# Kernel tuning notes

Measured on AMD Instinct MI355X. Metric: run time of the kernel, lower is better.

Reference implementation:

```python
import jax, jax.numpy as jnp
import numpy as np

N_TOK, BATCH, D, MEM, H, W = 196, 64, 256, 2048, 16, 16


def setup_inputs() -> dict:
    key = jax.random.key(0)
    ks = jax.random.split(key, 9)
    w_scale = 1.0 / np.sqrt(D)  # ~ Linear default init scale
    return {
        "input_tokens": jax.random.normal(ks[0], (N_TOK, BATCH, D), jnp.float32),
        "ch_memory": jax.random.normal(ks[1], (MEM, D), jnp.float32) * 0.1,
        "ch_wq": jax.random.normal(ks[2], (D, D), jnp.float32) * w_scale,
        "ch_wk": jax.random.normal(ks[3], (D, D), jnp.float32) * w_scale,
        "ch_wv": jax.random.normal(ks[4], (D, D), jnp.float32) * w_scale,
        "sp_memory": jax.random.normal(ks[5], (MEM, H, W), jnp.float32) * 0.1,
        "sp_wq": jax.random.normal(ks[6], (D, D), jnp.float32) * w_scale,
        "sp_wk": jax.random.normal(ks[7], (D, D), jnp.float32) * w_scale,
        "sp_wv": jax.random.normal(ks[8], (D, D), jnp.float32) * w_scale,
    }


def reference(input_tokens, ch_memory, ch_wq, ch_wk, ch_wv,
              sp_memory, sp_wq, sp_wk, sp_wv):
    n_tok, batch, d = input_tokens.shape
    hw = d  # spatial branch requires feature_dim == H*W
    x = input_tokens.reshape(n_tok * batch, d)  # [NB, D]

    # ---- Channel memory branch: dot-product softmax read ----
    q = x @ ch_wq.T                       # [NB, D]
    k = ch_memory @ ch_wk.T               # [M, D]
    v = ch_memory @ ch_wv.T               # [M, D]
    scores = (q @ k.T) * (1.0 / jnp.sqrt(jnp.float32(d)))  # [NB, M]
    att_c = jax.nn.softmax(scores, axis=-1)
    out_c = att_c @ v                     # [NB, D]

    # ---- Spatial memory branch: SSIM-score softmax read ----
    mem_flat = sp_memory.reshape(sp_memory.shape[0], hw)  # [M, HW]
    qf = x @ sp_wq.T                      # [NB, HW]
    kf = mem_flat @ sp_wk.T               # [M, HW]
    vf = mem_flat @ sp_wv.T               # [M, HW]

    q_mean = jnp.mean(qf, axis=1, keepdims=True)          # [NB, 1]
    k_mean = jnp.mean(kf, axis=1, keepdims=True)          # [M, 1]
    q_var = jnp.var(qf, axis=1, ddof=1, keepdims=True)    # unbiased, like torch.var
    k_var = jnp.var(kf, axis=1, ddof=1, keepdims=True)
    cov = ((qf - q_mean) @ (kf - k_mean).T) / jnp.float32(hw - 1)  # [NB, M]

    c1, c2 = 0.01, 0.03
    mean_prod = q_mean @ k_mean.T                          # [NB, M]
    numerator = (2.0 * mean_prod + c1) * (2.0 * cov + c2)
    denominator = (q_mean ** 2 + (k_mean.T) ** 2 + c1) * (q_var + k_var.T + c2)
    ssim = numerator / (denominator + 1e-8)                # [NB, M]

    att_s = jax.nn.softmax(ssim, axis=-1)
    out_s = att_s @ vf                     # [NB, HW] == [NB, D]

    return (out_c + out_s).reshape(n_tok, batch, d)
```

## Files before the change

### kernel.cpp

```cpp
#include <hip/hip_runtime.h>

#define NBQ 12544
#define DM  256
#define MM  2048

typedef __attribute__((ext_vector_type(8)))  __bf16 bf16x8;
typedef __attribute__((ext_vector_type(4)))  float  floatx4;

__device__ __forceinline__ ushort f2bf(float x) {
    unsigned u = __float_as_uint(x);
    u += 0x7fffu + ((u >> 16) & 1u);
    return (ushort)(u >> 16);
}
__device__ __forceinline__ float bf2f(ushort h) {
    return __uint_as_float(((unsigned)h) << 16);
}

__device__ __forceinline__ void glds16(const ushort* g, ushort* l) {
    __builtin_amdgcn_global_load_lds(
        (const __attribute__((address_space(1))) unsigned int*)g,
        (__attribute__((address_space(3))) unsigned int*)l, 16, 0, 0);
}

__global__ __launch_bounds__(256) void gemm_proj_all(
    const float* __restrict__ x,      const float* __restrict__ ch_mem,
    const float* __restrict__ ch_wq,  const float* __restrict__ ch_wk,
    const float* __restrict__ ch_wv,  const float* __restrict__ sp_mem,
    const float* __restrict__ sp_wq,  const float* __restrict__ sp_wk,
    const float* __restrict__ sp_wv,
    ushort* __restrict__ Qb,  ushort* __restrict__ QFb,
    ushort* __restrict__ Kb,  ushort* __restrict__ KFb,
    ushort* __restrict__ Vtb, ushort* __restrict__ VFtb)
{
    __shared__ ushort As[64][72];
    __shared__ ushort W1s[64][72];
    __shared__ ushort W2s[64][72];

    int bid = blockIdx.x;
    const float* A; const float* W1; const float* W2;
    ushort* C1; ushort* C2; int nrows, trans2;
    if (bid < 784) {
        A = x; W1 = ch_wq; W2 = sp_wq; C1 = Qb; C2 = QFb; nrows = NBQ; trans2 = 0;
    } else if (bid < 912) {
        A = ch_mem; W1 = ch_wk; W2 = ch_wv; C1 = Kb; C2 = Vtb;
        nrows = MM; trans2 = 1; bid -= 784;
    } else {
        A = sp_mem; W1 = sp_wk; W2 = sp_wv; C1 = KFb; C2 = VFtb;
        nrows = MM; trans2 = 1; bid -= 912;
    }
    const int r0 = (bid >> 2) * 64;
    const int c0 = (bid & 3) * 64;

    const int tid  = threadIdx.x;
    const int wv   = tid >> 6;
    const int lane = tid & 63;
    const int quad = lane >> 4;
    const int l16  = lane & 15;
    const int rw = (wv & 1) * 32;
    const int cw = (wv >> 1) * 32;

    floatx4 acc1[2][2], acc2[2][2];
    #pragma unroll
    for (int i = 0; i < 2; ++i)
        #pragma unroll
        for (int j = 0; j < 2; ++j) {
            acc1[i][j] = (floatx4){0.f, 0.f, 0.f, 0.f};
            acc2[i][j] = (floatx4){0.f, 0.f, 0.f, 0.f};
        }

    float4 a4[4], w14[4], w24[4];
    #pragma unroll
    for (int it = 0; it < 4; ++it) {
        int idx = tid + it * 256;
        int r = idx >> 4, c4 = (idx & 15) * 4;
        a4[it]  = *(const float4*)(A  + (size_t)(r0 + r) * 256 + c4);
        w14[it] = *(const float4*)(W1 + (size_t)(c0 + r) * 256 + c4);
        w24[it] = *(const float4*)(W2 + (size_t)(c0 + r) * 256 + c4);
    }

    for (int d0 = 0; d0 < 256; d0 += 64) {
        __syncthreads();
        #pragma unroll
        for (int it = 0; it < 4; ++it) {
            int idx = tid + it * 256;
            int r = idx >> 4, c4 = (idx & 15) * 4;
            ushort4 ab, w1b, w2b;
            ab.x = f2bf(a4[it].x);  ab.y = f2bf(a4[it].y);  ab.z = f2bf(a4[it].z);  ab.w = f2bf(a4[it].w);
            w1b.x = f2bf(w14[it].x); w1b.y = f2bf(w14[it].y); w1b.z = f2bf(w14[it].z); w1b.w = f2bf(w14[it].w);
            w2b.x = f2bf(w24[it].x); w2b.y = f2bf(w24[it].y); w2b.z = f2bf(w24[it].z); w2b.w = f2bf(w24[it].w);
            *(ushort4*)&As[r][c4]  = ab;
            *(ushort4*)&W1s[r][c4] = w1b;
            *(ushort4*)&W2s[r][c4] = w2b;
        }
        if (d0 + 64 < 256) {
            #pragma unroll
            for (int it = 0; it < 4; ++it) {
                int idx = tid + it * 256;
                int r = idx >> 4, c4 = (idx & 15) * 4;
                a4[it]  = *(const float4*)(A  + (size_t)(r0 + r) * 256 + d0 + 64 + c4);
                w14[it] = *(const float4*)(W1 + (size_t)(c0 + r) * 256 + d0 + 64 + c4);
                w24[it] = *(const float4*)(W2 + (size_t)(c0 + r) * 256 + d0 + 64 + c4);
            }
        }
        __syncthreads();
        #pragma unroll
        for (int kk = 0; kk < 64; kk += 32) {
            bf16x8 aA0 = *(const bf16x8*)&As[rw + l16][kk + quad * 8];
            bf16x8 aA1 = *(const bf16x8*)&As[rw + 16 + l16][kk + quad * 8];
            bf16x8 b10 = *(const bf16x8*)&W1s[cw + l16][kk + quad * 8];
            bf16x8 b11 = *(const bf16x8*)&W1s[cw + 16 + l16][kk + quad * 8];
            bf16x8 b20 = *(const bf16x8*)&W2s[cw + l16][kk + quad * 8];
            bf16x8 b21 = *(const bf16x8*)&W2s[cw + 16 + l16][kk + quad * 8];
            acc1[0][0] = __builtin_amdgcn_mfma_f32_16x16x32_bf16(aA0, b10, acc1[0][0], 0, 0, 0);
            acc1[0][1] = __builtin_amdgcn_mfma_f32_16x16x32_bf16(aA0, b11, acc1[0][1], 0, 0, 0);
            acc1[1][0] = __builtin_amdgcn_mfma_f32_16x16x32_bf16(aA1, b10, acc1[1][0], 0, 0, 0);
            acc1[1][1] = __builtin_amdgcn_mfma_f32_16x16x32_bf16(aA1, b11, acc1[1][1], 0, 0, 0);
            acc2[0][0] = __builtin_amdgcn_mfma_f32_16x16x32_bf16(aA0, b20, acc2[0][0], 0, 0, 0);
            acc2[0][1] = __builtin_amdgcn_mfma_f32_16x16x32_bf16(aA0, b21, acc2[0][1], 0, 0, 0);
            acc2[1][0] = __builtin_amdgcn_mfma_f32_16x16x32_bf16(aA1, b20, acc2[1][0], 0, 0, 0);
            acc2[1][1] = __builtin_amdgcn_mfma_f32_16x16x32_bf16(aA1, b21, acc2[1][1], 0, 0, 0);
        }
    }

    #pragma unroll
    for (int ag = 0; ag < 2; ++ag)
        #pragma unroll
        for (int cg = 0; cg < 2; ++cg)
            #pragma unroll
            for (int i = 0; i < 4; ++i)
                C1[(size_t)(r0 + rw + ag * 16 + quad * 4 + i) * 256
                   + c0 + cw + cg * 16 + l16] = f2bf(acc1[ag][cg][i]);

    if (!trans2) {
        #pragma unroll
        for (int ag = 0; ag < 2; ++ag)
            #pragma unroll
            for (int cg = 0; cg < 2; ++cg)
                #pragma unroll
                for (int i = 0; i < 4; ++i)
                    C2[(size_t)(r0 + rw + ag * 16 + quad * 4 + i) * 256
                       + c0 + cw + cg * 16 + l16] = f2bf(acc2[ag][cg][i]);
    } else {
        __syncthreads();
        #pragma unroll
        for (int ag = 0; ag < 2; ++ag)
            #pragma unroll
            for (int cg = 0; cg < 2; ++cg)
                #pragma unroll
                for (int i = 0; i < 4; ++i)
                    W2s[cw + cg * 16 + l16][rw + ag * 16 + quad * 4 + i] = f2bf(acc2[ag][cg][i]);
        __syncthreads();
        const int col = tid >> 2;
        const int seg = (tid & 3) * 16;
        #pragma unroll
        for (int j = 0; j < 2; ++j)
            *(uint4*)(C2 + (size_t)(c0 + col) * nrows + r0 + seg + j * 8) =
                *(const uint4*)&W2s[col][seg + j * 8];
    }
}

__global__ __launch_bounds__(256) void row_stats_kf(
    const ushort* __restrict__ KFb, float* __restrict__ km, float* __restrict__ kv)
{
    const int row  = blockIdx.x * 4 + (threadIdx.x >> 6);
    const int lane = threadIdx.x & 63;
    ushort4 u = *(const ushort4*)(KFb + (size_t)row * 256 + lane * 4);
    float a = bf2f(u.x), b = bf2f(u.y), c = bf2f(u.z), d = bf2f(u.w);
    float s  = a + b + c + d;
    float ss = a * a + b * b + c * c + d * d;
    #pragma unroll
    for (int off = 32; off > 0; off >>= 1) {
        s  += __shfl_down(s, off);
        ss += __shfl_down(ss, off);
    }
    if (lane == 0) {
        float m = s * (1.f / 256.f);
        km[row] = m;
        kv[row] = (ss - 256.f * m * m) * (1.f / 255.f);
    }
}

#define STAGE_TILE(b, ti)                                                     \
    {                                                                         \
        const ushort* kp_ = kp0 + (size_t)(ti) * 32 * DM;                     \
        const ushort* vp_ = vp0 + (ti) * 32;                                  \
        ushort* dst_ = SMu + (b) * 16384;                                     \
        _Pragma("unroll")                                                     \
        for (int p = 0; p < 4; ++p) {                                         \
            int db = (wv * 4 + p) * 512;                                      \
            glds16(kp_ + offK[p], dst_ + db);                                 \
            glds16(vp_ + offV[p], dst_ + 8192 + db);                          \
        }                                                                     \
    }

template<int NHALF>
__global__ __launch_bounds__(256, 2) void fused_attn_1br(
    const ushort* __restrict__ Qb,  const ushort* __restrict__ QFb,
    const ushort* __restrict__ Kb,  const ushort* __restrict__ KFb,
    const ushort* __restrict__ Vtb, const ushort* __restrict__ VFtb,
    const float* __restrict__ km_, const float* __restrict__ kv_,
    float* __restrict__ part, float* __restrict__ denp)
{
    __shared__ ushort SMu[32768];

    const int tid  = threadIdx.x;
    const int wv   = tid >> 6;
    const int lane = tid & 63;
    const int quad = lane >> 4;
    const int l16  = lane & 15;

    const int NQC = NBQ / 128;
    const int per_br = NQC * NHALF;
    int bid = blockIdx.x;
    const int br  = (bid < per_br) ? 1 : 0;
    int rem = br ? bid : bid - per_br;
    const int half = rem / NQC;
    const int qc   = rem - half * NQC;
    const int q0   = qc * 128;
    const int kbase = half * (MM / NHALF);
    const int NT   = (MM / NHALF) / 32;

    const ushort* qsrc = br ? QFb : Qb;
    const ushort* Ksel = br ? KFb : Kb;
    const ushort* Vsel = br ? VFtb : Vtb;

    bf16x8 aQ0[8], aQ1[8];
    {
        const ushort* qp = qsrc + (size_t)(q0 + wv * 32 + l16) * DM + quad * 8;
        #pragma unroll
        for (int s = 0; s < 8; ++s) {
            aQ0[s] = *(const bf16x8*)(qp + s * 32);
            aQ1[s] = *(const bf16x8*)(qp + 16 * DM + s * 32);
        }
    }

    float qmv0 = 0.f, qvv0 = 0.f, qmv1 = 0.f, qvv1 = 0.f;
    if (br) {
        float s0 = 0.f, ss0 = 0.f, s1 = 0.f, ss1 = 0.f;
        #pragma unroll
        for (int s = 0; s < 8; ++s)
            #pragma unroll
            for (int j = 0; j < 8; ++j) {
                float v0 = (float)aQ0[s][j], v1 = (float)aQ1[s][j];
                s0 += v0; ss0 += v0 * v0; s1 += v1; ss1 += v1 * v1;
            }
        s0  += __shfl_xor(s0, 16, 64);  s0  += __shfl_xor(s0, 32, 64);
        ss0 += __shfl_xor(ss0, 16, 64); ss0 += __shfl_xor(ss0, 32, 64);
        s1  += __shfl_xor(s1, 16, 64);  s1  += __shfl_xor(s1, 32, 64);
        ss1 += __shfl_xor(ss1, 16, 64); ss1 += __shfl_xor(ss1, 32, 64);
        qmv0 = s0 * (1.f / 256.f);
        qvv0 = (ss0 - 256.f * qmv0 * qmv0) * (1.f / 255.f);
        qmv1 = s1 * (1.f / 256.f);
        qvv1 = (ss1 - 256.f * qmv1 * qmv1) * (1.f / 255.f);
    }

    int offK[4], offV[4];
    #pragma unroll
    for (int p = 0; p < 4; ++p) {
        int j  = wv * 4 + p;
        int Rk = 2 * j + (lane >> 5);
        int rk = (Rk & 3) + ((Rk >> 4) & 1) * 4 + ((Rk >> 2) & 3) * 8;
        int ck = (lane & 31) ^ (Rk & 7);
        offK[p] = rk * DM + ck * 8;
        int Rv = 16 * j + (lane >> 2);
        int cv = (lane & 3) ^ (Rv & 3);
        offV[p] = Rv * MM + cv * 8;
    }

    const ushort* kp0 = Ksel + (size_t)kbase * DM;
    const ushort* vp0 = Vsel + kbase;

    floatx4 acc0[16], acc1[16];
    #pragma unroll
    for (int t = 0; t < 16; ++t) {
        acc0[t] = (floatx4){0.f, 0.f, 0.f, 0.f};
        acc1[t] = (floatx4){0.f, 0.f, 0.f, 0.f};
    }
    float den0 = 0.f, den1 = 0.f;
    const int ksw  = l16 & 7;
    const int vswo = (quad ^ (l16 & 3)) * 8;

    STAGE_TILE(0, 0);
    __syncthreads();

    int buf = 0;
    for (int ti = 0; ti < NT; ++ti) {
        if (ti + 1 < NT) STAGE_TILE(buf ^ 1, ti + 1);

        const ushort* Ks = SMu + buf * 16384;
        const ushort* Vs = Ks + 8192;

        floatx4 S00 = (floatx4){0.f, 0.f, 0.f, 0.f};
        floatx4 S10 = (floatx4){0.f, 0.f, 0.f, 0.f};
        floatx4 S01 = (floatx4){0.f, 0.f, 0.f, 0.f};
        floatx4 S11 = (floatx4){0.f, 0.f, 0.f, 0.f};
        #pragma unroll
        for (int s = 0; s < 8; ++s) {
            int off = ((s * 4 + quad) ^ ksw) * 8;
            bf16x8 aK0 = *(const bf16x8*)(Ks + l16 * DM + off);
            bf16x8 aK1 = *(const bf16x8*)(Ks + 4096 + l16 * DM + off);
            S00 = __builtin_amdgcn_mfma_f32_16x16x32_bf16(aK0, aQ0[s], S00, 0, 0, 0);
            S10 = __builtin_amdgcn_mfma_f32_16x16x32_bf16(aK1, aQ0[s], S10, 0, 0, 0);
            S01 = __builtin_amdgcn_mfma_f32_16x16x32_bf16(aK0, aQ1[s], S01, 0, 0, 0);
            S11 = __builtin_amdgcn_mfma_f32_16x16x32_bf16(aK1, aQ1[s], S11, 0, 0, 0);
        }

        const int kk = kbase + ti * 32;
        float p0[8], p1[8];
        if (!br) {
            #pragma unroll
            for (int r = 0; r < 4; ++r) {
                p0[r]     = __expf(S00[r] * 0.0625f);
                p0[4 + r] = __expf(S10[r] * 0.0625f);
                p1[r]     = __expf(S01[r] * 0.0625f);
                p1[4 + r] = __expf(S11[r] * 0.0625f);
            }
        } else {
            floatx4 km0 = *(const floatx4*)(km_ + kk + 8 * quad);
            floatx4 km1 = *(const floatx4*)(km_ + kk + 8 * quad + 4);
            floatx4 kv0 = *(const floatx4*)(kv_ + kk + 8 * quad);
            floatx4 kv1 = *(const floatx4*)(kv_ + kk + 8 * quad + 4);
            #pragma unroll
            for (int r = 0; r < 4; ++r) {
                {
                    float mp  = qmv0 * km0[r];
                    float cov = (S00[r] - 256.f * mp) * (1.f / 255.f);
                    float num = (2.f * mp + 0.01f) * (2.f * cov + 0.03f);
                    float dn  = (qmv0 * qmv0 + km0[r] * km0[r] + 0.01f) * (qvv0 + kv0[r] + 0.03f);
                    p0[r] = __expf(num / (dn + 1e-8f));
                }
                {
                    float mp  = qmv0 * km1[r];
                    float cov = (S10[r] - 256.f * mp) * (1.f / 255.f);
                    float num = (2.f * mp + 0.01f) * (2.f * cov + 0.03f);
                    float dn  = (qmv0 * qmv0 + km1[r] * km1[r] + 0.01f) * (qvv0 + kv1[r] + 0.03f);
                    p0[4 + r] = __expf(num / (dn + 1e-8f));
                }
                {
                    float mp  = qmv1 * km0[r];
                    float cov = (S01[r] - 256.f * mp) * (1.f / 255.f);
                    float num = (2.f * mp + 0.01f) * (2.f * cov + 0.03f);
                    float dn  = (qmv1 * qmv1 + km0[r] * km0[r] + 0.01f) * (qvv1 + kv0[r] + 0.03f);
                    p1[r] = __expf(num / (dn + 1e-8f));
                }
                {
                    float mp  = qmv1 * km1[r];
                    float cov = (S11[r] - 256.f * mp) * (1.f / 255.f);
                    float num = (2.f * mp + 0.01f) * (2.f * cov + 0.03f);
                    float dn  = (qmv1 * qmv1 + km1[r] * km1[r] + 0.01f) * (qvv1 + kv1[r] + 0.03f);
                    p1[4 + r] = __expf(num / (dn + 1e-8f));
                }
            }
        }
        union { ushort u[8]; bf16x8 v; } ap0, ap1;
        #pragma unroll
        for (int j = 0; j < 8; ++j) {
            den0 += p0[j]; ap0.u[j] = f2bf(p0[j]);
            den1 += p1[j]; ap1.u[j] = f2bf(p1[j]);
        }

        #pragma unroll
        for (int t = 0; t < 16; ++t) {
            bf16x8 bV = *(const bf16x8*)(Vs + (t * 16 + l16) * 32 + vswo);
            acc0[t] = __builtin_amdgcn_mfma_f32_16x16x32_bf16(ap0.v, bV, acc0[t], 0, 0, 0);
            acc1[t] = __builtin_amdgcn_mfma_f32_16x16x32_bf16(ap1.v, bV, acc1[t], 0, 0, 0);
        }

        __syncthreads();
        buf ^= 1;
    }

    den0 += __shfl_xor(den0, 16, 64); den0 += __shfl_xor(den0, 32, 64);
    den1 += __shfl_xor(den1, 16, 64); den1 += __shfl_xor(den1, 32, 64);

    const int sec = br * NHALF + half;
    float* Np = part + (size_t)sec * ((size_t)NBQ * DM);
    #pragma unroll
    for (int t = 0; t < 16; ++t)
        #pragma unroll
        for (int r = 0; r < 4; ++r) {
            int row = q0 + wv * 32 + quad * 4 + r;
            Np[(size_t)row * DM + t * 16 + l16]        = acc0[t][r];
            Np[(size_t)(row + 16) * DM + t * 16 + l16] = acc1[t][r];
        }
    if (lane < 16) {
        denp[(size_t)sec * NBQ + q0 + wv * 32 + lane]      = den0;
        denp[(size_t)sec * NBQ + q0 + wv * 32 + 16 + lane] = den1;
    }
}

__global__ __launch_bounds__(256, 2) void fused_attn_fb(
    const ushort* __restrict__ Qb,  const ushort* __restrict__ QFb,
    const ushort* __restrict__ Kb,  const ushort* __restrict__ KFb,
    const ushort* __restrict__ Vtb, const ushort* __restrict__ VFtb,
    const float* __restrict__ km_, const float* __restrict__ kv_,
    float* __restrict__ out)
{
    __shared__ ushort SMu[32768];
    float* combuf = (float*)SMu;

    const int tid  = threadIdx.x;
    const int wv   = tid >> 6;
    const int lane = tid & 63;
    const int quad = lane >> 4;
    const int l16  = lane & 15;
    const int qsel = wv & 1;
    const int br   = wv >> 1;
    const int q0   = blockIdx.x * 32;

    const ushort* qsrc = br ? QFb : Qb;
    bf16x8 aQ[8];
    {
        const ushort* qp = qsrc + (size_t)(q0 + qsel * 16 + l16) * DM + quad * 8;
        #pragma unroll
        for (int s = 0; s < 8; ++s) aQ[s] = *(const bf16x8*)(qp + s * 32);
    }

    float qmv = 0.f, qvv = 0.f;
    if (br) {
        float sum = 0.f, ss = 0.f;
        #pragma unroll
        for (int s = 0; s < 8; ++s)
            #pragma unroll
            for (int j = 0; j < 8; ++j) {
                float v = (float)aQ[s][j];
                sum += v; ss += v * v;
            }
        sum += __shfl_xor(sum, 16, 64); sum += __shfl_xor(sum, 32, 64);
        ss  += __shfl_xor(ss, 16, 64);  ss  += __shfl_xor(ss, 32, 64);
        qmv = sum * (1.f / 256.f);
        qvv = (ss - 256.f * qmv * qmv) * (1.f / 255.f);
    }

    int offK[4], offV[4];
    #pragma unroll
    for (int p = 0; p < 4; ++p) {
        int j  = wv * 4 + p;
        int Rk = 2 * j + (lane >> 5);
        int rk = (Rk & 3) + ((Rk >> 4) & 1) * 4 + ((Rk >> 2) & 3) * 8;
        int ck = (lane & 31) ^ (Rk & 7);
        offK[p] = rk * DM + ck * 8;
        int Rv = 16 * j + (lane >> 2);
        int cv = (lane & 3) ^ (Rv & 3);
        offV[p] = Rv * MM + cv * 8;
    }

    const ushort* kp  = Kb;
    const ushort* kfp = KFb;
    const ushort* vp  = Vtb;
    const ushort* vfp = VFtb;

    floatx4 acc[16];
    #pragma unroll
    for (int t = 0; t < 16; ++t) acc[t] = (floatx4){0.f, 0.f, 0.f, 0.f};
    float den = 0.f;

    const int ksw  = l16 & 7;
    const int vswo = (quad ^ (l16 & 3)) * 8;

    for (int kt = 0; kt < MM; kt += 32) {
        __syncthreads();
        #pragma unroll
        for (int p = 0; p < 4; ++p) {
            int db = (wv * 4 + p) * 512;
            glds16(kp  + offK[p], SMu + db);
            glds16(kfp + offK[p], SMu + 4096 + db);
            glds16(vp  + offV[p], SMu + 16384 + db);
            glds16(vfp + offV[p], SMu + 24576 + db);
        }
        kp += 32 * DM; kfp += 32 * DM; vp += 32; vfp += 32;
        __syncthreads();

        const ushort* Ks = SMu + (br ? 4096 : 0);
        floatx4 S0 = (floatx4){0.f, 0.f, 0.f, 0.f};
        floatx4 S1 = (floatx4){0.f, 0.f, 0.f, 0.f};
        #pragma unroll
        for (int s = 0; s < 8; ++s) {
            int off = ((s * 4 + quad) ^ ksw) * 8;
            bf16x8 aK0 = *(const bf16x8*)(Ks + l16 * DM + off);
            bf16x8 aK1 = *(const bf16x8*)(Ks + 2048 + l16 * DM + off);
            S0 = __builtin_amdgcn_mfma_f32_16x16x32_bf16(aK0, aQ[s], S0, 0, 0, 0);
            S1 = __builtin_amdgcn_mfma_f32_16x16x32_bf16(aK1, aQ[s], S1, 0, 0, 0);
        }

        float pb[8];
        if (!br) {
            #pragma unroll
            for (int r = 0; r < 4; ++r) {
                pb[r]     = __expf(S0[r] * 0.0625f);
                pb[4 + r] = __expf(S1[r] * 0.0625f);
            }
        } else {
            floatx4 km0 = *(const floatx4*)(km_ + kt + 8 * quad);
            floatx4 km1 = *(const floatx4*)(km_ + kt + 8 * quad + 4);
            floatx4 kv0 = *(const floatx4*)(kv_ + kt + 8 * quad);
            floatx4 kv1 = *(const floatx4*)(kv_ + kt + 8 * quad + 4);
            #pragma unroll
            for (int r = 0; r < 4; ++r) {
                {
                    float mp  = qmv * km0[r];
                    float cov = (S0[r] - 256.f * mp) * (1.f / 255.f);
                    float num = (2.f * mp + 0.01f) * (2.f * cov + 0.03f);
                    float dn  = (qmv * qmv + km0[r] * km0[r] + 0.01f) * (qvv + kv0[r] + 0.03f);
                    pb[r] = __expf(num / (dn + 1e-8f));
                }
                {
                    float mp  = qmv * km1[r];
                    float cov = (S1[r] - 256.f * mp) * (1.f / 255.f);
                    float num = (2.f * mp + 0.01f) * (2.f * cov + 0.03f);
                    float dn  = (qmv * qmv + km1[r] * km1[r] + 0.01f) * (qvv + kv1[r] + 0.03f);
                    pb[4 + r] = __expf(num / (dn + 1e-8f));
                }
            }
        }
        union { ushort u[8]; bf16x8 v; } ap;
        #pragma unroll
        for (int j = 0; j < 8; ++j) {
            den += pb[j];
            ap.u[j] = f2bf(pb[j]);
        }

        const ushort* Vs = SMu + (br ? 24576 : 16384);
        #pragma unroll
        for (int t = 0; t < 16; ++t) {
            bf16x8 bV = *(const bf16x8*)(Vs + (t * 16 + l16) * 32 + vswo);
            acc[t] = __builtin_amdgcn_mfma_f32_16x16x32_bf16(ap.v, bV, acc[t], 0, 0, 0);
        }
    }

    den += __shfl_xor(den, 16, 64);
    den += __shfl_xor(den, 32, 64);
    float rdn[4];
    #pragma unroll
    for (int r = 0; r < 4; ++r)
        rdn[r] = 1.f / __shfl(den, quad * 4 + r, 64);

    __syncthreads();
    if (br) {
        #pragma unroll
        for (int t = 0; t < 16; ++t)
            #pragma unroll
            for (int r = 0; r < 4; ++r)
                combuf[(qsel * 16 + quad * 4 + r) * 256 + t * 16 + l16] = acc[t][r] * rdn[r];
    }
    __syncthreads();
    if (!br) {
        #pragma unroll
        for (int t = 0; t < 16; ++t)
            #pragma unroll
            for (int r = 0; r < 4; ++r) {
                int ql = qsel * 16 + quad * 4 + r;
                out[(size_t)(q0 + ql) * DM + t * 16 + l16] =
                    acc[t][r] * rdn[r] + combuf[ql * 256 + t * 16 + l16];
            }
    }
}

template<int NH>
__global__ __launch_bounds__(256) void combine_halves(
    const float* __restrict__ part, const float* __restrict__ denp,
    float* __restrict__ out)
{
    const size_t stride = (size_t)NBQ * 64;
    const float4* p4 = (const float4*)part;
    float4* o4 = (float4*)out;
    #pragma unroll
    for (int u = 0; u < 2; ++u) {
        size_t i = (size_t)blockIdx.x * 512 + (size_t)u * 256 + threadIdx.x;
        int q = (int)(i >> 6);
        float dc = 0.f, ds = 0.f;
        #pragma unroll
        for (int h = 0; h < NH; ++h) {
            dc += denp[(size_t)h * NBQ + q];
            ds += denp[(size_t)(NH + h) * NBQ + q];
        }
        float rc = 1.f / dc, rs = 1.f / ds;
        float4 nc = {0.f, 0.f, 0.f, 0.f}, ns = {0.f, 0.f, 0.f, 0.f};
        #pragma unroll
        for (int h = 0; h < NH; ++h) {
            float4 c = p4[(size_t)h * stride + i];
            float4 s = p4[(size_t)(NH + h) * stride + i];
            nc.x += c.x; nc.y += c.y; nc.z += c.z; nc.w += c.w;
            ns.x += s.x; ns.y += s.y; ns.z += s.z; ns.w += s.w;
        }
        float4 r;
        r.x = nc.x * rc + ns.x * rs;
        r.y = nc.y * rc + ns.y * rs;
        r.z = nc.z * rc + ns.z * rs;
        r.w = nc.w * rc + ns.w * rs;
        o4[i] = r;
    }
}

extern "C" void kernel_launch(void* const* d_in, const int* in_sizes, int n_in,
                              void* d_out, int out_size, void* d_ws, size_t ws_size,
                              hipStream_t stream)
{
    const float* x      = (const float*)d_in[0];
    const float* ch_mem = (const float*)d_in[1];
    const float* ch_wq  = (const float*)d_in[2];
    const float* ch_wk  = (const float*)d_in[3];
    const float* ch_wv  = (const float*)d_in[4];
    const float* sp_mem = (const float*)d_in[5];
    const float* sp_wq  = (const float*)d_in[6];
    const float* sp_wk  = (const float*)d_in[7];
    const float* sp_wv  = (const float*)d_in[8];
    float* out = (float*)d_out;

    ushort* Qb   = (ushort*)d_ws;
    ushort* QFb  = Qb   + (size_t)NBQ * DM;
    ushort* Kb   = QFb  + (size_t)NBQ * DM;
    ushort* KFb  = Kb   + (size_t)MM * DM;
    ushort* Vtb  = KFb  + (size_t)MM * DM;
    ushort* VFtb = Vtb  + (size_t)MM * DM;
    float*  km   = (float*)(VFtb + (size_t)MM * DM);
    float*  kv   = km + MM;
    float*  denp = kv + MM;
    float*  part = denp + (size_t)8 * NBQ;

    const size_t base_b = (size_t)((char*)part - (char*)d_ws);
    const size_t need4  = base_b + (size_t)8 * NBQ * DM * sizeof(float);
    const size_t need2  = base_b + (size_t)4 * NBQ * DM * sizeof(float);

    dim3 blk(256);
    gemm_proj_all<<<dim3(1040), blk, 0, stream>>>(
        x, ch_mem, ch_wq, ch_wk, ch_wv, sp_mem, sp_wq, sp_wk, sp_wv,
        Qb, QFb, Kb, KFb, Vtb, VFtb);
    row_stats_kf<<<dim3(MM / 4), blk, 0, stream>>>(KFb, km, kv);
    if (ws_size >= need4) {
        fused_attn_1br<4><<<dim3(2 * (NBQ / 128) * 4), blk, 0, stream>>>(
            Qb, QFb, Kb, KFb, Vtb, VFtb, km, kv, part, denp);
        combine_halves<4><<<dim3(NBQ * DM / 4 / 512), blk, 0, stream>>>(part, denp, out);
    } else if (ws_size >= need2) {
        fused_attn_1br<2><<<dim3(2 * (NBQ / 128) * 2), blk, 0, stream>>>(
            Qb, QFb, Kb, KFb, Vtb, VFtb, km, kv, part, denp);
        combine_halves<2><<<dim3(NBQ * DM / 4 / 512), blk, 0, stream>>>(part, denp, out);
    } else {
        fused_attn_fb<<<dim3(NBQ / 32), blk, 0, stream>>>(
            Qb, QFb, Kb, KFb, Vtb, VFtb, km, kv, out);
    }
}
```

Measured before the change: 258.2 us.

## Pipeline attention tiles with explicit vmcnt waits and remap blocks for locality

The fused attention kernel is specialized to four key splits. Its block index is remapped so the eight blocks sharing a query chunk or key slice are adjacent. The full __syncthreads is replaced by counted s_waitcnt vmcnt waits plus raw s_barrier, so the next tile's async LDS loads overlap compute, and km/kv are prefetched one tile ahead. It also folds the SSIM constants into precomputed terms (c2 moved into kv, c1 into q mean squared), uses hardware bf16 conversion, and adds nontemporal loads and stores for Q and the partial buffers. The hand-written wait counts depend on the exact number of outstanding loads and could break silently if that changes. The fallback kernel's LDS offsets are also changed.

```diff
diff --git a/kernel.cpp b/kernel.cpp
--- a/kernel.cpp
+++ b/kernel.cpp
@@ -15,12 +15,21 @@
 __device__ __forceinline__ float bf2f(ushort h) {
     return __uint_as_float(((unsigned)h) << 16);
 }
+__device__ __forceinline__ ushort4 cvt4(float4 f) {
+    union { __bf16 h[4]; ushort4 u; } r;
+    r.h[0] = (__bf16)f.x; r.h[1] = (__bf16)f.y;
+    r.h[2] = (__bf16)f.z; r.h[3] = (__bf16)f.w;
+    return r.u;
+}
 
 __device__ __forceinline__ void glds16(const ushort* g, ushort* l) {
     __builtin_amdgcn_global_load_lds(
         (const __attribute__((address_space(1))) unsigned int*)g,
         (__attribute__((address_space(3))) unsigned int*)l, 16, 0, 0);
 }
+
+#define WAITVM(N) asm volatile("s_waitcnt vmcnt(" #N ")" ::: "memory")
+#define WAITLGKM0 asm volatile("s_waitcnt lgkmcnt(0)" ::: "memory")
 
 __global__ __launch_bounds__(256) void gemm_proj_all(
     const float* __restrict__ x,      const float* __restrict__ ch_mem,
@@ -84,13 +93,9 @@
         for (int it = 0; it < 4; ++it) {
             int idx = tid + it * 256;
             int r = idx >> 4, c4 = (idx & 15) * 4;
-            ushort4 ab, w1b, w2b;
-            ab.x = f2bf(a4[it].x);  ab.y = f2bf(a4[it].y);  ab.z = f2bf(a4[it].z);  ab.w = f2bf(a4[it].w);
-            w1b.x = f2bf(w14[it].x); w1b.y = f2bf(w14[it].y); w1b.z = f2bf(w14[it].z); w1b.w = f2bf(w14[it].w);
-            w2b.x = f2bf(w24[it].x); w2b.y = f2bf(w24[it].y); w2b.z = f2bf(w24[it].z); w2b.w = f2bf(w24[it].w);
-            *(ushort4*)&As[r][c4]  = ab;
-            *(ushort4*)&W1s[r][c4] = w1b;
-            *(ushort4*)&W2s[r][c4] = w2b;
+            *(ushort4*)&As[r][c4]  = cvt4(a4[it]);
+            *(ushort4*)&W1s[r][c4] = cvt4(w14[it]);
+            *(ushort4*)&W2s[r][c4] = cvt4(w24[it]);
         }
         if (d0 + 64 < 256) {
             #pragma unroll
@@ -176,7 +181,7 @@
     if (lane == 0) {
         float m = s * (1.f / 256.f);
         km[row] = m;
-        kv[row] = (ss - 256.f * m * m) * (1.f / 255.f);
+        kv[row] = (ss - 256.f * m * m) * (1.f / 255.f) + 0.03f;
     }
 }
 
@@ -193,8 +198,7 @@
         }                                                                     \
     }
 
-template<int NHALF>
-__global__ __launch_bounds__(256, 2) void fused_attn_1br(
+__global__ __launch_bounds__(256, 2) void fused_attn_x4(
     const ushort* __restrict__ Qb,  const ushort* __restrict__ QFb,
     const ushort* __restrict__ Kb,  const ushort* __restrict__ KFb,
     const ushort* __restrict__ Vtb, const ushort* __restrict__ VFtb,
@@ -209,16 +213,14 @@
     const int quad = lane >> 4;
     const int l16  = lane & 15;
 
-    const int NQC = NBQ / 128;
-    const int per_br = NQC * NHALF;
-    int bid = blockIdx.x;
-    const int br  = (bid < per_br) ? 1 : 0;
-    int rem = br ? bid : bid - per_br;
-    const int half = rem / NQC;
-    const int qc   = rem - half * NQC;
+    const int k8   = blockIdx.x & 7;
+    const int j    = blockIdx.x >> 3;
+    const int br   = (j >= 49) ? 1 : 0;
+    const int half = k8 & 3;
+    const int qc   = (k8 >> 2) * 49 + (br ? j - 49 : j);
     const int q0   = qc * 128;
-    const int kbase = half * (MM / NHALF);
-    const int NT   = (MM / NHALF) / 32;
+    const int kbase = half * 512;
+    const int NT   = 16;
 
     const ushort* qsrc = br ? QFb : Qb;
     const ushort* Ksel = br ? KFb : Kb;
@@ -229,19 +231,19 @@
         const ushort* qp = qsrc + (size_t)(q0 + wv * 32 + l16) * DM + quad * 8;
         #pragma unroll
         for (int s = 0; s < 8; ++s) {
-            aQ0[s] = *(const bf16x8*)(qp + s * 32);
-            aQ1[s] = *(const bf16x8*)(qp + 16 * DM + s * 32);
-        }
-    }
-
-    float qmv0 = 0.f, qvv0 = 0.f, qmv1 = 0.f, qvv1 = 0.f;
+            aQ0[s] = __builtin_nontemporal_load((const bf16x8*)(qp + s * 32));
+            aQ1[s] = __builtin_nontemporal_load((const bf16x8*)(qp + 16 * DM + s * 32));
+        }
+    }
+
+    float qmv0 = 0.f, qvv0 = 0.f, qmv1 = 0.f, qvv1 = 0.f, qm2_0 = 0.f, qm2_1 = 0.f;
     if (br) {
         float s0 = 0.f, ss0 = 0.f, s1 = 0.f, ss1 = 0.f;
         #pragma unroll
         for (int s = 0; s < 8; ++s)
             #pragma unroll
-            for (int j = 0; j < 8; ++j) {
-                float v0 = (float)aQ0[s][j], v1 = (float)aQ1[s][j];
+            for (int jj = 0; jj < 8; ++jj) {
+                float v0 = (float)aQ0[s][jj], v1 = (float)aQ1[s][jj];
                 s0 += v0; ss0 += v0 * v0; s1 += v1; ss1 += v1 * v1;
             }
         s0  += __shfl_xor(s0, 16, 64);  s0  += __shfl_xor(s0, 32, 64);
@@ -252,17 +254,19 @@
         qvv0 = (ss0 - 256.f * qmv0 * qmv0) * (1.f / 255.f);
         qmv1 = s1 * (1.f / 256.f);
         qvv1 = (ss1 - 256.f * qmv1 * qmv1) * (1.f / 255.f);
+        qm2_0 = qmv0 * qmv0 + 0.01f;
+        qm2_1 = qmv1 * qmv1 + 0.01f;
     }
 
     int offK[4], offV[4];
     #pragma unroll
     for (int p = 0; p < 4; ++p) {
-        int j  = wv * 4 + p;
-        int Rk = 2 * j + (lane >> 5);
+        int jw = wv * 4 + p;
+        int Rk = 2 * jw + (lane >> 5);
         int rk = (Rk & 3) + ((Rk >> 4) & 1) * 4 + ((Rk >> 2) & 3) * 8;
         int ck = (lane & 31) ^ (Rk & 7);
         offK[p] = rk * DM + ck * 8;
-        int Rv = 16 * j + (lane >> 2);
+        int Rv = 16 * jw + (lane >> 2);
         int cv = (lane & 3) ^ (Rv & 3);
         offV[p] = Rv * MM + cv * 8;
     }
@@ -280,12 +284,35 @@
     const int ksw  = l16 & 7;
     const int vswo = (quad ^ (l16 & 3)) * 8;
 
+    floatx4 kmc0 = {0,0,0,0}, kmc1 = {0,0,0,0}, kvc0 = {0,0,0,0}, kvc1 = {0,0,0,0};
+
     STAGE_TILE(0, 0);
-    __syncthreads();
+    if (br) {
+        kmc0 = *(const floatx4*)(km_ + kbase + 8 * quad);
+        kmc1 = *(const floatx4*)(km_ + kbase + 8 * quad + 4);
+        kvc0 = *(const floatx4*)(kv_ + kbase + 8 * quad);
+        kvc1 = *(const floatx4*)(kv_ + kbase + 8 * quad + 4);
+    }
 
     int buf = 0;
     for (int ti = 0; ti < NT; ++ti) {
-        if (ti + 1 < NT) STAGE_TILE(buf ^ 1, ti + 1);
+        const bool have_next = (ti + 1 < NT);
+        floatx4 kmn0 = {0,0,0,0}, kmn1 = {0,0,0,0}, kvn0 = {0,0,0,0}, kvn1 = {0,0,0,0};
+        if (have_next) {
+            STAGE_TILE(buf ^ 1, ti + 1);
+            if (br) {
+                const int kk1 = kbase + (ti + 1) * 32;
+                kmn0 = *(const floatx4*)(km_ + kk1 + 8 * quad);
+                kmn1 = *(const floatx4*)(km_ + kk1 + 8 * quad + 4);
+                kvn0 = *(const floatx4*)(kv_ + kk1 + 8 * quad);
+                kvn1 = *(const floatx4*)(kv_ + kk1 + 8 * quad + 4);
+            }
+        }
+        if (have_next) { if (br) WAITVM(12); else WAITVM(8); }
+        else           { WAITVM(0); }
+        __builtin_amdgcn_sched_barrier(0);
+        __builtin_amdgcn_s_barrier();
+        __builtin_amdgcn_sched_barrier(0);
 
         const ushort* Ks = SMu + buf * 16384;
         const ushort* Vs = Ks + 8192;
@@ -305,7 +332,6 @@
             S11 = __builtin_amdgcn_mfma_f32_16x16x32_bf16(aK1, aQ1[s], S11, 0, 0, 0);
         }
 
-        const int kk = kbase + ti * 32;
         float p0[8], p1[8];
         if (!br) {
             #pragma unroll
@@ -316,47 +342,47 @@
                 p1[4 + r] = __expf(S11[r] * 0.0625f);
             }
         } else {
-            floatx4 km0 = *(const floatx4*)(km_ + kk + 8 * quad);
-            floatx4 km1 = *(const floatx4*)(km_ + kk + 8 * quad + 4);
-            floatx4 kv0 = *(const floatx4*)(kv_ + kk + 8 * quad);
-            floatx4 kv1 = *(const floatx4*)(kv_ + kk + 8 * quad + 4);
             #pragma unroll
             for (int r = 0; r < 4; ++r) {
                 {
-                    float mp  = qmv0 * km0[r];
+                    float kmr = kmc0[r];
+                    float mp  = qmv0 * kmr;
                     float cov = (S00[r] - 256.f * mp) * (1.f / 255.f);
                     float num = (2.f * mp + 0.01f) * (2.f * cov + 0.03f);
-                    float dn  = (qmv0 * qmv0 + km0[r] * km0[r] + 0.01f) * (qvv0 + kv0[r] + 0.03f);
-                    p0[r] = __expf(num / (dn + 1e-8f));
+                    float dn  = (qm2_0 + kmr * kmr) * (qvv0 + kvc0[r]) + 1e-8f;
+                    p0[r] = __expf(num / dn);
                 }
                 {
-                    float mp  = qmv0 * km1[r];
+                    float kmr = kmc1[r];
+                    float mp  = qmv0 * kmr;
                     float cov = (S10[r] - 256.f * mp) * (1.f / 255.f);
                     float num = (2.f * mp + 0.01f) * (2.f * cov + 0.03f);
-                    float dn  = (qmv0 * qmv0 + km1[r] * km1[r] + 0.01f) * (qvv0 + kv1[r] + 0.03f);
-                    p0[4 + r] = __expf(num / (dn + 1e-8f));
+                    float dn  = (qm2_0 + kmr * kmr) * (qvv0 + kvc1[r]) + 1e-8f;
+                    p0[4 + r] = __expf(num / dn);
                 }
                 {
-                    float mp  = qmv1 * km0[r];
+                    float kmr = kmc0[r];
+                    float mp  = qmv1 * kmr;
                     float cov = (S01[r] - 256.f * mp) * (1.f / 255.f);
                     float num = (2.f * mp + 0.01f) * (2.f * cov + 0.03f);
-                    float dn  = (qmv1 * qmv1 + km0[r] * km0[r] + 0.01f) * (qvv1 + kv0[r] + 0.03f);
-                    p1[r] = __expf(num / (dn + 1e-8f));
+                    float dn  = (qm2_1 + kmr * kmr) * (qvv1 + kvc0[r]) + 1e-8f;
+                    p1[r] = __expf(num / dn);
                 }
                 {
-                    float mp  = qmv1 * km1[r];
+                    float kmr = kmc1[r];
+                    float mp  = qmv1 * kmr;
                     float cov = (S11[r] - 256.f * mp) * (1.f / 255.f);
                     float num = (2.f * mp + 0.01f) * (2.f * cov + 0.03f);
-                    float dn  = (qmv1 * qmv1 + km1[r] * km1[r] + 0.01f) * (qvv1 + kv1[r] + 0.03f);
-                    p1[4 + r] = __expf(num / (dn + 1e-8f));
+                    float dn  = (qm2_1 + kmr * kmr) * (qvv1 + kvc1[r]) + 1e-8f;
+                    p1[4 + r] = __expf(num / dn);
                 }
             }
         }
-        union { ushort u[8]; bf16x8 v; } ap0, ap1;
-        #pragma unroll
-        for (int j = 0; j < 8; ++j) {
-            den0 += p0[j]; ap0.u[j] = f2bf(p0[j]);
-            den1 += p1[j]; ap1.u[j] = f2bf(p1[j]);
+        union { __bf16 h[8]; bf16x8 v; } ap0, ap1;
+        #pragma unroll
+        for (int jj = 0; jj < 8; ++jj) {
+            den0 += p0[jj]; ap0.h[jj] = (__bf16)p0[jj];
+            den1 += p1[jj]; ap1.h[jj] = (__bf16)p1[jj];
         }
 
         #pragma unroll
@@ -366,22 +392,27 @@
             acc1[t] = __builtin_amdgcn_mfma_f32_16x16x32_bf16(ap1.v, bV, acc1[t], 0, 0, 0);
         }
 
-        __syncthreads();
+        WAITLGKM0;
+        __builtin_amdgcn_sched_barrier(0);
+        __builtin_amdgcn_s_barrier();
+        __builtin_amdgcn_sched_barrier(0);
+
+        kmc0 = kmn0; kmc1 = kmn1; kvc0 = kvn0; kvc1 = kvn1;
         buf ^= 1;
     }
 
     den0 += __shfl_xor(den0, 16, 64); den0 += __shfl_xor(den0, 32, 64);
     den1 += __shfl_xor(den1, 16, 64); den1 += __shfl_xor(den1, 32, 64);
 
-    const int sec = br * NHALF + half;
+    const int sec = br * 4 + half;
     float* Np = part + (size_t)sec * ((size_t)NBQ * DM);
     #pragma unroll
     for (int t = 0; t < 16; ++t)
         #pragma unroll
         for (int r = 0; r < 4; ++r) {
             int row = q0 + wv * 32 + quad * 4 + r;
-            Np[(size_t)row * DM + t * 16 + l16]        = acc0[t][r];
-            Np[(size_t)(row + 16) * DM + t * 16 + l16] = acc1[t][r];
+            __builtin_nontemporal_store(acc0[t][r], &Np[(size_t)row * DM + t * 16 + l16]);
+            __builtin_nontemporal_store(acc1[t][r], &Np[(size_t)(row + 16) * DM + t * 16 + l16]);
         }
     if (lane < 16) {
         denp[(size_t)sec * NBQ + q0 + wv * 32 + lane]      = den0;
@@ -416,31 +447,32 @@
         for (int s = 0; s < 8; ++s) aQ[s] = *(const bf16x8*)(qp + s * 32);
     }
 
-    float qmv = 0.f, qvv = 0.f;
+    float qmv = 0.f, qvv = 0.f, qm2 = 0.f;
     if (br) {
         float sum = 0.f, ss = 0.f;
         #pragma unroll
         for (int s = 0; s < 8; ++s)
             #pragma unroll
-            for (int j = 0; j < 8; ++j) {
-                float v = (float)aQ[s][j];
+            for (int jj = 0; jj < 8; ++jj) {
+                float v = (float)aQ[s][jj];
                 sum += v; ss += v * v;
             }
         sum += __shfl_xor(sum, 16, 64); sum += __shfl_xor(sum, 32, 64);
         ss  += __shfl_xor(ss, 16, 64);  ss  += __shfl_xor(ss, 32, 64);
         qmv = sum * (1.f / 256.f);
         qvv = (ss - 256.f * qmv * qmv) * (1.f / 255.f);
+        qm2 = qmv * qmv + 0.01f;
     }
 
     int offK[4], offV[4];
     #pragma unroll
     for (int p = 0; p < 4; ++p) {
-        int j  = wv * 4 + p;
-        int Rk = 2 * j + (lane >> 5);
+        int jw = wv * 4 + p;
+        int Rk = 2 * jw + (lane >> 5);
         int rk = (Rk & 3) + ((Rk >> 4) & 1) * 4 + ((Rk >> 2) & 3) * 8;
         int ck = (lane & 31) ^ (Rk & 7);
         offK[p] = rk * DM + ck * 8;
-        int Rv = 16 * j + (lane >> 2);
+        int Rv = 16 * jw + (lane >> 2);
         int cv = (lane & 3) ^ (Rv & 3);
         offV[p] = Rv * MM + cv * 8;
     }
@@ -464,21 +496,21 @@
         for (int p = 0; p < 4; ++p) {
             int db = (wv * 4 + p) * 512;
             glds16(kp  + offK[p], SMu + db);
-            glds16(kfp + offK[p], SMu + 4096 + db);
+            glds16(kfp + offK[p], SMu + 8192 + db);
             glds16(vp  + offV[p], SMu + 16384 + db);
             glds16(vfp + offV[p], SMu + 24576 + db);
         }
         kp += 32 * DM; kfp += 32 * DM; vp += 32; vfp += 32;
         __syncthreads();
 
-        const ushort* Ks = SMu + (br ? 4096 : 0);
+        const ushort* Ks = SMu + (br ? 8192 : 0);
         floatx4 S0 = (floatx4){0.f, 0.f, 0.f, 0.f};
         floatx4 S1 = (floatx4){0.f, 0.f, 0.f, 0.f};
         #pragma unroll
         for (int s = 0; s < 8; ++s) {
             int off = ((s * 4 + quad) ^ ksw) * 8;
             bf16x8 aK0 = *(const bf16x8*)(Ks + l16 * DM + off);
-            bf16x8 aK1 = *(const bf16x8*)(Ks + 2048 + l16 * DM + off);
+            bf16x8 aK1 = *(const bf16x8*)(Ks + 4096 + l16 * DM + off);
             S0 = __builtin_amdgcn_mfma_f32_16x16x32_bf16(aK0, aQ[s], S0, 0, 0, 0);
             S1 = __builtin_amdgcn_mfma_f32_16x16x32_bf16(aK1, aQ[s], S1, 0, 0, 0);
         }
@@ -498,26 +530,28 @@
             #pragma unroll
             for (int r = 0; r < 4; ++r) {
                 {
-                    float mp  = qmv * km0[r];
+                    float kmr = km0[r];
+                    float mp  = qmv * kmr;
                     float cov = (S0[r] - 256.f * mp) * (1.f / 255.f);
                     float num = (2.f * mp + 0.01f) * (2.f * cov + 0.03f);
-                    float dn  = (qmv * qmv + km0[r] * km0[r] + 0.01f) * (qvv + kv0[r] + 0.03f);
-                    pb[r] = __expf(num / (dn + 1e-8f));
+                    float dn  = (qm2 + kmr * kmr) * (qvv + kv0[r]) + 1e-8f;
+                    pb[r] = __expf(num / dn);
                 }
                 {
-                    float mp  = qmv * km1[r];
+                    float kmr = km1[r];
+                    float mp  = qmv * kmr;
                     float cov = (S1[r] - 256.f * mp) * (1.f / 255.f);
                     float num = (2.f * mp + 0.01f) * (2.f * cov + 0.03f);
-                    float dn  = (qmv * qmv + km1[r] * km1[r] + 0.01f) * (qvv + kv1[r] + 0.03f);
-                    pb[4 + r] = __expf(num / (dn + 1e-8f));
+                    float dn  = (qm2 + kmr * kmr) * (qvv + kv1[r]) + 1e-8f;
+                    pb[4 + r] = __expf(num / dn);
                 }
             }
         }
-        union { ushort u[8]; bf16x8 v; } ap;
-        #pragma unroll
-        for (int j = 0; j < 8; ++j) {
-            den += pb[j];
-            ap.u[j] = f2bf(pb[j]);
+        union { __bf16 h[8]; bf16x8 v; } ap;
+        #pragma unroll
+        for (int jj = 0; jj < 8; ++jj) {
+            den += pb[jj];
+            ap.h[jj] = (__bf16)pb[jj];
         }
 
         const ushort* Vs = SMu + (br ? 24576 : 16384);
@@ -556,39 +590,33 @@
     }
 }
 
-template<int NH>
 __global__ __launch_bounds__(256) void combine_halves(
     const float* __restrict__ part, const float* __restrict__ denp,
     float* __restrict__ out)
 {
     const size_t stride = (size_t)NBQ * 64;
-    const float4* p4 = (const float4*)part;
-    float4* o4 = (float4*)out;
+    const floatx4* p4 = (const floatx4*)part;
+    floatx4* o4 = (floatx4*)out;
     #pragma unroll
     for (int u = 0; u < 2; ++u) {
         size_t i = (size_t)blockIdx.x * 512 + (size_t)u * 256 + threadIdx.x;
         int q = (int)(i >> 6);
         float dc = 0.f, ds = 0.f;
         #pragma unroll
-        for (int h = 0; h < NH; ++h) {
+        for (int h = 0; h < 4; ++h) {
             dc += denp[(size_t)h * NBQ + q];
-            ds += denp[(size_t)(NH + h) * NBQ + q];
+            ds += denp[(size_t)(4 + h) * NBQ + q];
         }
         float rc = 1.f / dc, rs = 1.f / ds;
-        float4 nc = {0.f, 0.f, 0.f, 0.f}, ns = {0.f, 0.f, 0.f, 0.f};
-        #pragma unroll
-        for (int h = 0; h < NH; ++h) {
-            float4 c = p4[(size_t)h * stride + i];
-            float4 s = p4[(size_t)(NH + h) * stride + i];
-            nc.x += c.x; nc.y += c.y; nc.z += c.z; nc.w += c.w;
-            ns.x += s.x; ns.y += s.y; ns.z += s.z; ns.w += s.w;
-        }
-        float4 r;
-        r.x = nc.x * rc + ns.x * rs;
-        r.y = nc.y * rc + ns.y * rs;
-        r.z = nc.z * rc + ns.z * rs;
-        r.w = nc.w * rc + ns.w * rs;
-        o4[i] = r;
+        floatx4 nc = {0.f, 0.f, 0.f, 0.f}, ns = {0.f, 0.f, 0.f, 0.f};
+        #pragma unroll
+        for (int h = 0; h < 4; ++h) {
+            floatx4 c = __builtin_nontemporal_load(&p4[(size_t)h * stride + i]);
+            floatx4 s = __builtin_nontemporal_load(&p4[(size_t)(4 + h) * stride + i]);
+            nc += c;
+            ns += s;
+        }
+        o4[i] = nc * rc + ns * rs;
     }
 }
 
@@ -620,7 +648,6 @@
 
     const size_t base_b = (size_t)((char*)part - (char*)d_ws);
     const size_t need4  = base_b + (size_t)8 * NBQ * DM * sizeof(float);
-    const size_t need2  = base_b + (size_t)4 * NBQ * DM * sizeof(float);
 
     dim3 blk(256);
     gemm_proj_all<<<dim3(1040), blk, 0, stream>>>(
@@ -628,13 +655,9 @@
         Qb, QFb, Kb, KFb, Vtb, VFtb);
     row_stats_kf<<<dim3(MM / 4), blk, 0, stream>>>(KFb, km, kv);
     if (ws_size >= need4) {
-        fused_attn_1br<4><<<dim3(2 * (NBQ / 128) * 4), blk, 0, stream>>>(
+        fused_attn_x4<<<dim3(784), blk, 0, stream>>>(
             Qb, QFb, Kb, KFb, Vtb, VFtb, km, kv, part, denp);
-        combine_halves<4><<<dim3(NBQ * DM / 4 / 512), blk, 0, stream>>>(part, denp, out);
-    } else if (ws_size >= need2) {
-        fused_attn_1br<2><<<dim3(2 * (NBQ / 128) * 2), blk, 0, stream>>>(
-            Qb, QFb, Kb, KFb, Vtb, VFtb, km, kv, part, denp);
-        combine_halves<2><<<dim3(NBQ * DM / 4 / 512), blk, 0, stream>>>(part, denp, out);
+        combine_halves<<<dim3(NBQ * DM / 4 / 512), blk, 0, stream>>>(part, denp, out);
     } else {
         fused_attn_fb<<<dim3(NBQ / 32), blk, 0, stream>>>(
             Qb, QFb, Kb, KFb, Vtb, VFtb, km, kv, out);
```

New measurement: 306.7 us. 18.8% more time.
